# Kernel tuning notes

Hardware: AMD Instinct MI355X
Metric: run time of the kernel (lower is better)

The kernel has to match this reference:

```python
import jax, jax.numpy as jnp
import numpy as np

N_EMBD = 1024
N_HEAD = 16
HEAD_SIZE = N_EMBD // N_HEAD  # 64


def setup_inputs() -> dict:
    key = jax.random.key(0)
    k1, k2, k3, k4 = jax.random.split(key, 4)
    B, T = 4, 4096
    x = jax.random.normal(k1, (B, T, N_EMBD), dtype=jnp.float32)
    scale = 1.0 / np.sqrt(N_EMBD)
    # Linear(n_embd, head_size, bias=False): store as [C, H] so projection is x @ W
    Wk = jax.random.normal(k2, (N_EMBD, HEAD_SIZE), dtype=jnp.float32) * scale
    Wq = jax.random.normal(k3, (N_EMBD, HEAD_SIZE), dtype=jnp.float32) * scale
    Wv = jax.random.normal(k4, (N_EMBD, HEAD_SIZE), dtype=jnp.float32) * scale
    decay_factor = jnp.array([-0.5], dtype=jnp.float32)
    return {"x": x, "Wk": Wk, "Wq": Wq, "Wv": Wv, "decay_factor": decay_factor}


def reference(x, Wk, Wq, Wv, decay_factor):
    B, T, C = x.shape
    H = Wk.shape[1]
    k = x @ Wk  # [B,T,H]
    q = x @ Wq  # [B,T,H]
    v = x @ Wv  # [B,T,H]
    wei = jnp.einsum('bth,bsh->bts', q, k) * (H ** -0.5)  # [B,T,T]
    idx = jnp.arange(T)
    dist = jnp.minimum(idx[None, :] - idx[:, None], 0)  # j - i, clamped max=0
    ripple_bias = dist.astype(x.dtype) * jnp.abs(decay_factor[0])
    wei = wei + ripple_bias[None, :, :]
    causal = idx[None, :] <= idx[:, None]  # tril mask [T,T]
    wei = jnp.where(causal[None, :, :], wei, -jnp.inf)
    wei = jax.nn.softmax(wei, axis=-1)
    return jnp.einsum('bts,bsh->bth', wei, v)
```

## Files before the change

### kernel.cpp

```cpp
#include <hip/hip_runtime.h>

typedef short bf16x8 __attribute__((ext_vector_type(8)));
typedef float f32x4 __attribute__((ext_vector_type(4)));

#define TT 4096
#define CC 1024
#define HH 64
#define MTOT 16384

static __device__ __forceinline__ unsigned short f2bf(float f) {
  unsigned int u = __float_as_uint(f);
  unsigned int r = (u + 0x7FFFu + ((u >> 16) & 1u)) >> 16;
  return (unsigned short)r;
}

static __device__ __forceinline__ unsigned int pack_bf2(float lo, float hi) {
  unsigned int ul = __float_as_uint(lo) + 0x8000u;
  unsigned int uh = __float_as_uint(hi) + 0x8000u;
  return __builtin_amdgcn_perm(uh, ul, 0x07060302u);
}

typedef const __attribute__((address_space(1))) void gvoid;
typedef __attribute__((address_space(3))) void svoid;
static __device__ __forceinline__ void gll16(const void* g, void* l) {
  __builtin_amdgcn_global_load_lds((gvoid*)g, (svoid*)l, 16, 0, 0);
}

#define WAITVM(N) asm volatile("s_waitcnt vmcnt(" #N ")" ::: "memory")

__global__ void prep_wt(const float* __restrict__ Wk, const float* __restrict__ Wq,
                        const float* __restrict__ Wv, unsigned short* __restrict__ Wt) {
  __shared__ float T[64][65];
  const int mat = blockIdx.x >> 4;
  const int kt = blockIdx.x & 15;
  const float* src = (mat == 0) ? Wk : ((mat == 1) ? Wq : Wv);
#pragma unroll
  for (int i = 0; i < 4; ++i) {
    int c = i * 256 + threadIdx.x;
    int row = c >> 4, col = (c & 15) * 4;
    f32x4 v = *(const f32x4*)&src[(size_t)(kt * 64 + row) * HH + col];
    T[col + 0][row] = v[0];
    T[col + 1][row] = v[1];
    T[col + 2][row] = v[2];
    T[col + 3][row] = v[3];
  }
  __syncthreads();
#pragma unroll
  for (int i = 0; i < 2; ++i) {
    int c2 = i * 256 + threadIdx.x;
    int row = c2 >> 3, k0 = (c2 & 7) * 8;
    union { bf16x8 v; unsigned short h[8]; } pk;
#pragma unroll
    for (int j = 0; j < 8; ++j) pk.h[j] = f2bf(T[row][k0 + j]);
    *(bf16x8*)&Wt[(size_t)(mat * 64 + row) * CC + kt * 64 + k0] = pk.v;
  }
}

__global__ __launch_bounds__(512, 2) void proj_kernel(
    const float* __restrict__ x, const unsigned short* __restrict__ Wt,
    unsigned short* __restrict__ kb, unsigned short* __restrict__ qb,
    unsigned short* __restrict__ vt) {
  extern __shared__ __align__(16) char smem[];
  float* Xl = (float*)smem;
  unsigned short* Bl = (unsigned short*)(smem + 49152);

  const int tid = threadIdx.x;
  const int lane = tid & 63;
  const int w = tid >> 6;
  const int r = lane & 15, g = lane >> 4;
  const int rowgrp = w >> 1;
  const int colbase = (w & 1) * 96;
  const int m0 = blockIdx.x * 64;

  const float* xsrcs[2];
#pragma unroll
  for (int j = 0; j < 2; ++j) {
    int c = j * 512 + tid;
    int row = c >> 4, s = c & 15;
    xsrcs[j] = x + (size_t)(m0 + row) * CC + (((s & 8) | ((s & 7) ^ (row & 7))) * 4);
  }
  const unsigned short* bsrcs[3];
#pragma unroll
  for (int j = 0; j < 3; ++j) {
    int cb = j * 512 + tid;
    int row = cb >> 3, s = cb & 7;
    bsrcs[j] = Wt + (size_t)row * CC + ((s ^ (row & 7)) * 8);
  }

  f32x4 acc[6];
#pragma unroll
  for (int n = 0; n < 6; ++n) { f32x4 z = {0.f, 0.f, 0.f, 0.f}; acc[n] = z; }

  auto stage = [&](int t, int buf) {
    float* xb = Xl + buf * 4096;
    unsigned short* bb = Bl + buf * 12288;
#pragma unroll
    for (int j = 0; j < 2; ++j)
      gll16(xsrcs[j] + t * 64, xb + (j * 512 + w * 64) * 4);
#pragma unroll
    for (int j = 0; j < 3; ++j)
      gll16(bsrcs[j] + t * 64, bb + (size_t)(j * 512 + w * 64) * 8);
  };

  const int rr = rowgrp * 16 + r;
  const int rb = rr * 64;
  const int rx = rr & 7;

  auto body = [&](int buf) {
    const float* xb = Xl + buf * 4096;
    const unsigned short* bb = Bl + buf * 12288;
    bf16x8 bfr[2][6];
#pragma unroll
    for (int ks = 0; ks < 2; ++ks)
#pragma unroll
      for (int n = 0; n < 6; ++n) {
        int col = colbase + 16 * n + r;
        bfr[ks][n] = *(const bf16x8*)&bb[col * 64 + (((ks * 4 + g) ^ (col & 7)) * 8)];
      }
#pragma unroll
    for (int ks = 0; ks < 2; ++ks) {
      int s0 = ks * 8 + 2 * g;
      f32x4 v0 = *(const f32x4*)&xb[rb + (((s0 & 8) | ((s0 & 7) ^ rx)) * 4)];
      f32x4 v1 = *(const f32x4*)&xb[rb + ((((s0 + 1) & 8) | (((s0 + 1) & 7) ^ rx)) * 4)];
      union { bf16x8 v; unsigned int u[4]; } af;
      af.u[0] = pack_bf2(v0.x, v0.y);
      af.u[1] = pack_bf2(v0.z, v0.w);
      af.u[2] = pack_bf2(v1.x, v1.y);
      af.u[3] = pack_bf2(v1.z, v1.w);
#pragma unroll
      for (int n = 0; n < 6; ++n)
        acc[n] = __builtin_amdgcn_mfma_f32_16x16x32_bf16(af.v, bfr[ks][n], acc[n], 0, 0, 0);
    }
  };

  stage(0, 0);
  stage(1, 1);

  for (int t = 0; t < 15; ++t) {
    WAITVM(5);
    __builtin_amdgcn_s_barrier();
    if (t + 2 < 16) stage(t + 2, (t + 2) % 3);
    body(t % 3);
  }
  WAITVM(0);
  __builtin_amdgcn_s_barrier();
  body(0);

  float* Vt = (float*)(smem + 73728);
#pragma unroll
  for (int n = 0; n < 6; ++n) {
#pragma unroll
    for (int i = 0; i < 4; ++i) {
      int row = rowgrp * 16 + 4 * g + i;
      int col = colbase + 16 * n + r;
      float val = acc[n][i];
      if (col < 64) {
        kb[(size_t)(m0 + row) * HH + col] = f2bf(val);
      } else if (col < 128) {
        qb[(size_t)(m0 + row) * HH + (col - 64)] = f2bf(val);
      } else {
        Vt[(col - 128) * 65 + row] = val;
      }
    }
  }
  __syncthreads();
  {
    int dim = tid >> 3, t8 = (tid & 7) * 8;
    union { bf16x8 v; unsigned short h[8]; } pk;
#pragma unroll
    for (int j = 0; j < 8; ++j) pk.h[j] = f2bf(Vt[dim * 65 + t8 + j]);
    int b = m0 >> 12;
    int tt = (m0 & (TT - 1)) + t8;
    *(bf16x8*)&vt[(((size_t)b * HH + dim) << 12) + tt] = pk.v;
  }
}

__global__ __launch_bounds__(256, 2) void attn_kernel(
    const unsigned short* __restrict__ qb, const unsigned short* __restrict__ kb,
    const unsigned short* __restrict__ vt, const float* __restrict__ decayp,
    float* __restrict__ out) {
  extern __shared__ __align__(16) char smem[];
  unsigned short* Kl = (unsigned short*)smem;
  unsigned short* Vl = Kl + 16384;
  unsigned short* Pl = Vl + 16384;
  float* Ol = (float*)(smem + 65536);
  float* Ml = (float*)(smem + 65536 + 8704);
  float* Ll = Ml + 32;

  const int tid = threadIdx.x;
  const int lane = tid & 63;
  const int w = tid >> 6;
  const int r = lane & 15, g = lane >> 4;
  const int qh = w & 1;
  const int kvg = w >> 1;

  const int batch = blockIdx.x & 3;
  const int qt = blockIdx.x >> 2;
  const int qbase = qt * 32;
  const int qw = qbase + qh * 16;
  const int qrow = qw + r;

  const float decay = fabsf(decayp[0]);

  const unsigned short* qbb = qb + (size_t)batch * TT * HH;
  const unsigned short* kbb = kb + (size_t)batch * TT * HH;
  const unsigned short* vbb = vt + (size_t)batch * HH * TT;

  const unsigned short* qp = qbb + (size_t)qrow * HH;
  bf16x8 aq0 = *(const bf16x8*)(qp + 8 * g);
  bf16x8 aq1 = *(const bf16x8*)(qp + 32 + 8 * g);

  int t0 = 0;
  if (decay > 1e-8f) {
    float wf = 60.f / decay;
    if (wf < (float)TT) {
      int W = (int)wf + 1;
      int lo = qbase - W;
      if (lo < 0) lo = 0;
      t0 = lo >> 6;
    }
  }
  const int t1 = (qbase + 31) >> 6;
  const int nsteps = (t1 - t0 + 2) >> 1;

  const unsigned short* ksrc[4];
  const unsigned short* vsrc[4];
#pragma unroll
  for (int j = 0; j < 4; ++j) {
    int c = j * 256 + tid;
    int th = c >> 9;
    int cc = c & 511;
    int row = cc >> 3, sl = cc & 7;
    ksrc[j] = kbb + (size_t)((t0 + th) * 64 + row) * HH + ((sl ^ (row & 7)) * 8);
    vsrc[j] = vbb + (size_t)row * TT + (t0 + th) * 64 + ((sl ^ (row & 7)) * 8);
  }

  auto stage = [&](int s, int buf) {
#pragma unroll
    for (int j = 0; j < 4; ++j) {
      gll16(ksrc[j] + (size_t)s * 8192, Kl + buf * 8192 + (j * 256 + w * 64) * 8);
      gll16(vsrc[j] + s * 128, Vl + buf * 8192 + (j * 256 + w * 64) * 8);
    }
  };

  float m = -1e30f, lsum = 0.f;
  f32x4 o[4];
#pragma unroll
  for (int n = 0; n < 4; ++n) { f32x4 z = {0.f, 0.f, 0.f, 0.f}; o[n] = z; }

  stage(0, 0);

  for (int s = 0; s < nsteps; ++s) {
    if (s + 1 < nsteps) { stage(s + 1, (s + 1) & 1); WAITVM(8); }
    else { WAITVM(0); }
    __builtin_amdgcn_s_barrier();

    const int myt = t0 + 2 * s + kvg;
    if (myt <= t1) {
      const unsigned short* Kb = Kl + (s & 1) * 8192 + kvg * 4096;
      const unsigned short* Vb = Vl + (s & 1) * 8192 + kvg * 4096;
      const int kv0 = myt * 64;

      f32x4 sacc[4];
      __builtin_amdgcn_s_setprio(1);
#pragma unroll
      for (int t = 0; t < 4; ++t) {
        f32x4 z = {0.f, 0.f, 0.f, 0.f};
        int kvr = 16 * t + r;
        bf16x8 b0 = *(const bf16x8*)&Kb[kvr * 64 + ((g ^ (kvr & 7)) * 8)];
        bf16x8 b1 = *(const bf16x8*)&Kb[kvr * 64 + (((4 + g) ^ (kvr & 7)) * 8)];
        z = __builtin_amdgcn_mfma_f32_16x16x32_bf16(b0, aq0, z, 0, 0, 0);
        sacc[t] = __builtin_amdgcn_mfma_f32_16x16x32_bf16(b1, aq1, z, 0, 0, 0);
      }
      __builtin_amdgcn_s_setprio(0);

      float p[4][4];
      float rmax = -1e30f;
#pragma unroll
      for (int t = 0; t < 4; ++t)
#pragma unroll
        for (int i = 0; i < 4; ++i) {
          int kv = kv0 + 16 * t + 4 * g + i;
          float sv = sacc[t][i] * 0.125f + decay * (float)(kv - qrow);
          if (kv > qrow) sv = -1e30f;
          p[t][i] = sv;
          rmax = fmaxf(rmax, sv);
        }
      rmax = fmaxf(rmax, __shfl_xor(rmax, 16));
      rmax = fmaxf(rmax, __shfl_xor(rmax, 32));
      float mn = fmaxf(m, rmax);
      float al = __expf(m - mn);
      m = mn;
      float rs = 0.f;
#pragma unroll
      for (int t = 0; t < 4; ++t)
#pragma unroll
        for (int i = 0; i < 4; ++i) {
          float e = __expf(p[t][i] - mn);
          p[t][i] = e;
          rs += e;
        }
      rs += __shfl_xor(rs, 16);
      rs += __shfl_xor(rs, 32);
      lsum = lsum * al + rs;
#pragma unroll
      for (int n = 0; n < 4; ++n) {
        o[n][0] *= al; o[n][1] *= al; o[n][2] *= al; o[n][3] *= al;
      }

      char* P = (char*)(Pl + w * 1024) + r * 128;
#pragma unroll
      for (int t = 0; t < 4; ++t) {
        uint2 u;
        u.x = pack_bf2(p[t][0], p[t][1]);
        u.y = pack_bf2(p[t][2], p[t][3]);
        *(uint2*)(P + ((t ^ (r & 3)) * 32) + g * 8) = u;
      }
      bf16x8 pb0 = *(const bf16x8*)(P + (((g >> 1) ^ (r & 3)) * 32) + (g & 1) * 16);
      bf16x8 pb1 = *(const bf16x8*)(P + ((((g >> 1) + 2) ^ (r & 3)) * 32) + (g & 1) * 16);

      __builtin_amdgcn_s_setprio(1);
#pragma unroll
      for (int n = 0; n < 4; ++n) {
        int dim = 16 * n + r;
        bf16x8 v0 = *(const bf16x8*)&Vb[dim * 64 + ((g ^ (dim & 7)) * 8)];
        bf16x8 v1 = *(const bf16x8*)&Vb[dim * 64 + (((4 + g) ^ (dim & 7)) * 8)];
        o[n] = __builtin_amdgcn_mfma_f32_16x16x32_bf16(v0, pb0, o[n], 0, 0, 0);
        o[n] = __builtin_amdgcn_mfma_f32_16x16x32_bf16(v1, pb1, o[n], 0, 0, 0);
      }
      __builtin_amdgcn_s_setprio(0);
    }
    __builtin_amdgcn_s_barrier();
  }

  const int orow = qh * 16 + r;
  if (kvg == 1) {
    if (lane < 16) { Ml[orow] = m; Ll[orow] = lsum; }
#pragma unroll
    for (int n = 0; n < 4; ++n)
#pragma unroll
      for (int i = 0; i < 4; ++i)
        Ol[orow * 68 + 16 * n + 4 * g + i] = o[n][i];
  }
  __syncthreads();
  if (kvg == 0) {
    float m2 = Ml[orow], l2 = Ll[orow];
    float M = fmaxf(m, m2);
    float e1 = __expf(m - M), e2 = __expf(m2 - M);
    float inv = 1.f / (lsum * e1 + l2 * e2);
#pragma unroll
    for (int n = 0; n < 4; ++n)
#pragma unroll
      for (int i = 0; i < 4; ++i) {
        int d = 16 * n + 4 * g + i;
        Ol[orow * 68 + d] = (o[n][i] * e1 + Ol[orow * 68 + d] * e2) * inv;
      }
  }
  __syncthreads();

  float* ob = out + (size_t)batch * TT * HH;
#pragma unroll
  for (int j = 0; j < 2; ++j) {
    int c = j * 256 + tid;
    int row = c >> 4, q4 = (c & 15) * 4;
    f32x4 vv = *(const f32x4*)&Ol[row * 68 + q4];
    *(f32x4*)&ob[(size_t)(qbase + row) * HH + q4] = vv;
  }
}

extern "C" void kernel_launch(void* const* d_in, const int* in_sizes, int n_in,
                              void* d_out, int out_size, void* d_ws, size_t ws_size,
                              hipStream_t stream) {
  const float* x = (const float*)d_in[0];
  const float* Wk = (const float*)d_in[1];
  const float* Wq = (const float*)d_in[2];
  const float* Wv = (const float*)d_in[3];
  const float* decay = (const float*)d_in[4];
  float* out = (float*)d_out;

  unsigned short* kb = (unsigned short*)d_ws;
  unsigned short* qbw = kb + (size_t)MTOT * HH;
  unsigned short* vt = qbw + (size_t)MTOT * HH;
  unsigned short* Wt = vt + (size_t)MTOT * HH;

  prep_wt<<<dim3(48), dim3(256), 0, stream>>>(Wk, Wq, Wv, Wt);
  proj_kernel<<<dim3(256), dim3(512), 120 * 1024, stream>>>(x, Wt, kb, qbw, vt);
  attn_kernel<<<dim3(512), dim3(256), 74496, stream>>>(qbw, kb, vt, decay, out);
}
```

Baseline: 32.31 us.

## Fuse weight prep, projection and attention into one cooperative kernel

The three separate launches (weight transpose, QKV projection, attention) are merged into a single cooperative kernel with grid-wide syncs between phases. Each 512-thread block now runs two 256-thread attention units side by side instead of using 512 separate blocks. This removes launch overhead and inter-kernel gaps. In exchange, the attention K/V staging loses its double buffering: each step loads, waits for all loads and then syncs. Grid syncs add their own cost.

```diff
diff --git a/kernel.cpp b/kernel.cpp
--- a/kernel.cpp
+++ b/kernel.cpp
@@ -1,4 +1,7 @@
 #include <hip/hip_runtime.h>
+#include <hip/hip_cooperative_groups.h>
+
+namespace cg = cooperative_groups;
 
 typedef short bf16x8 __attribute__((ext_vector_type(8)));
 typedef float f32x4 __attribute__((ext_vector_type(4)));
@@ -28,343 +31,349 @@
 
 #define WAITVM(N) asm volatile("s_waitcnt vmcnt(" #N ")" ::: "memory")
 
-__global__ void prep_wt(const float* __restrict__ Wk, const float* __restrict__ Wq,
-                        const float* __restrict__ Wv, unsigned short* __restrict__ Wt) {
-  __shared__ float T[64][65];
-  const int mat = blockIdx.x >> 4;
-  const int kt = blockIdx.x & 15;
-  const float* src = (mat == 0) ? Wk : ((mat == 1) ? Wq : Wv);
-#pragma unroll
-  for (int i = 0; i < 4; ++i) {
-    int c = i * 256 + threadIdx.x;
-    int row = c >> 4, col = (c & 15) * 4;
-    f32x4 v = *(const f32x4*)&src[(size_t)(kt * 64 + row) * HH + col];
-    T[col + 0][row] = v[0];
-    T[col + 1][row] = v[1];
-    T[col + 2][row] = v[2];
-    T[col + 3][row] = v[3];
-  }
-  __syncthreads();
-#pragma unroll
-  for (int i = 0; i < 2; ++i) {
-    int c2 = i * 256 + threadIdx.x;
-    int row = c2 >> 3, k0 = (c2 & 7) * 8;
-    union { bf16x8 v; unsigned short h[8]; } pk;
-#pragma unroll
-    for (int j = 0; j < 8; ++j) pk.h[j] = f2bf(T[row][k0 + j]);
-    *(bf16x8*)&Wt[(size_t)(mat * 64 + row) * CC + kt * 64 + k0] = pk.v;
-  }
-}
-
-__global__ __launch_bounds__(512, 2) void proj_kernel(
-    const float* __restrict__ x, const unsigned short* __restrict__ Wt,
+__global__ __launch_bounds__(512, 2) void fused_kernel(
+    const float* __restrict__ x, const float* __restrict__ Wk,
+    const float* __restrict__ Wq, const float* __restrict__ Wv,
+    const float* __restrict__ decayp,
     unsigned short* __restrict__ kb, unsigned short* __restrict__ qb,
-    unsigned short* __restrict__ vt) {
+    unsigned short* __restrict__ vt, unsigned short* __restrict__ Wt,
+    float* __restrict__ out) {
   extern __shared__ __align__(16) char smem[];
-  float* Xl = (float*)smem;
-  unsigned short* Bl = (unsigned short*)(smem + 49152);
+  cg::grid_group grid = cg::this_grid();
 
   const int tid = threadIdx.x;
   const int lane = tid & 63;
   const int w = tid >> 6;
   const int r = lane & 15, g = lane >> 4;
-  const int rowgrp = w >> 1;
-  const int colbase = (w & 1) * 96;
-  const int m0 = blockIdx.x * 64;
-
-  const float* xsrcs[2];
-#pragma unroll
-  for (int j = 0; j < 2; ++j) {
-    int c = j * 512 + tid;
-    int row = c >> 4, s = c & 15;
-    xsrcs[j] = x + (size_t)(m0 + row) * CC + (((s & 8) | ((s & 7) ^ (row & 7))) * 4);
+
+  if (blockIdx.x < 48) {
+    float* T = (float*)smem;
+    const int mat = blockIdx.x >> 4;
+    const int kt = blockIdx.x & 15;
+    const float* src = (mat == 0) ? Wk : ((mat == 1) ? Wq : Wv);
+#pragma unroll
+    for (int i = 0; i < 2; ++i) {
+      int c = i * 512 + tid;
+      int row = c >> 4, col = (c & 15) * 4;
+      f32x4 v = *(const f32x4*)&src[(size_t)(kt * 64 + row) * HH + col];
+      T[(col + 0) * 65 + row] = v[0];
+      T[(col + 1) * 65 + row] = v[1];
+      T[(col + 2) * 65 + row] = v[2];
+      T[(col + 3) * 65 + row] = v[3];
+    }
+    __syncthreads();
+    {
+      int row = tid >> 3, k0 = (tid & 7) * 8;
+      union { bf16x8 v; unsigned short h[8]; } pk;
+#pragma unroll
+      for (int j = 0; j < 8; ++j) pk.h[j] = f2bf(T[row * 65 + k0 + j]);
+      *(bf16x8*)&Wt[(size_t)(mat * 64 + row) * CC + kt * 64 + k0] = pk.v;
+    }
   }
-  const unsigned short* bsrcs[3];
-#pragma unroll
-  for (int j = 0; j < 3; ++j) {
-    int cb = j * 512 + tid;
-    int row = cb >> 3, s = cb & 7;
-    bsrcs[j] = Wt + (size_t)row * CC + ((s ^ (row & 7)) * 8);
+  grid.sync();
+
+  {
+    float* Xl = (float*)smem;
+    unsigned short* Bl = (unsigned short*)(smem + 49152);
+
+    const int rowgrp = w >> 1;
+    const int colbase = (w & 1) * 96;
+    const int m0 = blockIdx.x * 64;
+
+    const float* xsrcs[2];
+#pragma unroll
+    for (int j = 0; j < 2; ++j) {
+      int c = j * 512 + tid;
+      int row = c >> 4, s = c & 15;
+      xsrcs[j] = x + (size_t)(m0 + row) * CC + (((s & 8) | ((s & 7) ^ (row & 7))) * 4);
+    }
+    const unsigned short* bsrcs[3];
+#pragma unroll
+    for (int j = 0; j < 3; ++j) {
+      int cb = j * 512 + tid;
+      int row = cb >> 3, s = cb & 7;
+      bsrcs[j] = Wt + (size_t)row * CC + ((s ^ (row & 7)) * 8);
+    }
+
+    f32x4 acc[6];
+#pragma unroll
+    for (int n = 0; n < 6; ++n) { f32x4 z = {0.f, 0.f, 0.f, 0.f}; acc[n] = z; }
+
+    auto stage = [&](int t, int buf) {
+      float* xb = Xl + buf * 4096;
+      unsigned short* bb = Bl + buf * 12288;
+#pragma unroll
+      for (int j = 0; j < 2; ++j)
+        gll16(xsrcs[j] + t * 64, xb + (j * 512 + w * 64) * 4);
+#pragma unroll
+      for (int j = 0; j < 3; ++j)
+        gll16(bsrcs[j] + t * 64, bb + (size_t)(j * 512 + w * 64) * 8);
+    };
+
+    const int rr = rowgrp * 16 + r;
+    const int rb = rr * 64;
+    const int rx = rr & 7;
+
+    auto body = [&](int buf) {
+      const float* xb = Xl + buf * 4096;
+      const unsigned short* bb = Bl + buf * 12288;
+      bf16x8 bfr[2][6];
+#pragma unroll
+      for (int ks = 0; ks < 2; ++ks)
+#pragma unroll
+        for (int n = 0; n < 6; ++n) {
+          int col = colbase + 16 * n + r;
+          bfr[ks][n] = *(const bf16x8*)&bb[col * 64 + (((ks * 4 + g) ^ (col & 7)) * 8)];
+        }
+#pragma unroll
+      for (int ks = 0; ks < 2; ++ks) {
+        int s0 = ks * 8 + 2 * g;
+        f32x4 v0 = *(const f32x4*)&xb[rb + (((s0 & 8) | ((s0 & 7) ^ rx)) * 4)];
+        f32x4 v1 = *(const f32x4*)&xb[rb + ((((s0 + 1) & 8) | (((s0 + 1) & 7) ^ rx)) * 4)];
+        union { bf16x8 v; unsigned int u[4]; } af;
+        af.u[0] = pack_bf2(v0.x, v0.y);
+        af.u[1] = pack_bf2(v0.z, v0.w);
+        af.u[2] = pack_bf2(v1.x, v1.y);
+        af.u[3] = pack_bf2(v1.z, v1.w);
+#pragma unroll
+        for (int n = 0; n < 6; ++n)
+          acc[n] = __builtin_amdgcn_mfma_f32_16x16x32_bf16(af.v, bfr[ks][n], acc[n], 0, 0, 0);
+      }
+    };
+
+    stage(0, 0);
+    stage(1, 1);
+
+    for (int t = 0; t < 15; ++t) {
+      WAITVM(5);
+      __builtin_amdgcn_s_barrier();
+      if (t + 2 < 16) stage(t + 2, (t + 2) % 3);
+      body(t % 3);
+    }
+    WAITVM(0);
+    __builtin_amdgcn_s_barrier();
+    body(0);
+
+    float* Vt = (float*)(smem + 73728);
+#pragma unroll
+    for (int n = 0; n < 6; ++n) {
+#pragma unroll
+      for (int i = 0; i < 4; ++i) {
+        int row = rowgrp * 16 + 4 * g + i;
+        int col = colbase + 16 * n + r;
+        float val = acc[n][i];
+        if (col < 64) {
+          kb[(size_t)(m0 + row) * HH + col] = f2bf(val);
+        } else if (col < 128) {
+          qb[(size_t)(m0 + row) * HH + (col - 64)] = f2bf(val);
+        } else {
+          Vt[(col - 128) * 65 + row] = val;
+        }
+      }
+    }
+    __syncthreads();
+    {
+      int dim = tid >> 3, t8 = (tid & 7) * 8;
+      union { bf16x8 v; unsigned short h[8]; } pk;
+#pragma unroll
+      for (int j = 0; j < 8; ++j) pk.h[j] = f2bf(Vt[dim * 65 + t8 + j]);
+      int b = m0 >> 12;
+      int tt = (m0 & (TT - 1)) + t8;
+      *(bf16x8*)&vt[(((size_t)b * HH + dim) << 12) + tt] = pk.v;
+    }
   }
-
-  f32x4 acc[6];
-#pragma unroll
-  for (int n = 0; n < 6; ++n) { f32x4 z = {0.f, 0.f, 0.f, 0.f}; acc[n] = z; }
-
-  auto stage = [&](int t, int buf) {
-    float* xb = Xl + buf * 4096;
-    unsigned short* bb = Bl + buf * 12288;
-#pragma unroll
-    for (int j = 0; j < 2; ++j)
-      gll16(xsrcs[j] + t * 64, xb + (j * 512 + w * 64) * 4);
-#pragma unroll
-    for (int j = 0; j < 3; ++j)
-      gll16(bsrcs[j] + t * 64, bb + (size_t)(j * 512 + w * 64) * 8);
-  };
-
-  const int rr = rowgrp * 16 + r;
-  const int rb = rr * 64;
-  const int rx = rr & 7;
-
-  auto body = [&](int buf) {
-    const float* xb = Xl + buf * 4096;
-    const unsigned short* bb = Bl + buf * 12288;
-    bf16x8 bfr[2][6];
-#pragma unroll
-    for (int ks = 0; ks < 2; ++ks)
-#pragma unroll
-      for (int n = 0; n < 6; ++n) {
-        int col = colbase + 16 * n + r;
-        bfr[ks][n] = *(const bf16x8*)&bb[col * 64 + (((ks * 4 + g) ^ (col & 7)) * 8)];
+  grid.sync();
+
+  {
+    unsigned short* KlA = (unsigned short*)smem;
+    unsigned short* VlA = (unsigned short*)(smem + 32768);
+    unsigned short* PlA = (unsigned short*)(smem + 65536);
+    float* OlA = (float*)(smem + 81920);
+    float* MlA = (float*)(smem + 99328);
+    float* LlA = (float*)(smem + 99584);
+
+    const int half = w >> 2;
+    const int wl = w & 3;
+    const int htid = tid & 255;
+    const int u = blockIdx.x * 2 + half;
+    const int batch = u & 3;
+    const int qt = u >> 2;
+    const int qbase = qt * 32;
+    const int qh = wl & 1;
+    const int kvg = wl >> 1;
+    const int qw = qbase + qh * 16;
+    const int qrow = qw + r;
+
+    const float decay = fabsf(decayp[0]);
+
+    const unsigned short* qbb = qb + (size_t)batch * TT * HH;
+    const unsigned short* kbb = kb + (size_t)batch * TT * HH;
+    const unsigned short* vbb = vt + (size_t)batch * HH * TT;
+
+    const unsigned short* qp = qbb + (size_t)qrow * HH;
+    bf16x8 aq0 = *(const bf16x8*)(qp + 8 * g);
+    bf16x8 aq1 = *(const bf16x8*)(qp + 32 + 8 * g);
+
+    int t0 = 0;
+    if (decay > 1e-8f) {
+      float wf = 60.f / decay;
+      if (wf < (float)TT) {
+        int W = (int)wf + 1;
+        int lo = qbase - W;
+        if (lo < 0) lo = 0;
+        t0 = lo >> 6;
       }
-#pragma unroll
-    for (int ks = 0; ks < 2; ++ks) {
-      int s0 = ks * 8 + 2 * g;
-      f32x4 v0 = *(const f32x4*)&xb[rb + (((s0 & 8) | ((s0 & 7) ^ rx)) * 4)];
-      f32x4 v1 = *(const f32x4*)&xb[rb + ((((s0 + 1) & 8) | (((s0 + 1) & 7) ^ rx)) * 4)];
-      union { bf16x8 v; unsigned int u[4]; } af;
-      af.u[0] = pack_bf2(v0.x, v0.y);
-      af.u[1] = pack_bf2(v0.z, v0.w);
-      af.u[2] = pack_bf2(v1.x, v1.y);
-      af.u[3] = pack_bf2(v1.z, v1.w);
-#pragma unroll
-      for (int n = 0; n < 6; ++n)
-        acc[n] = __builtin_amdgcn_mfma_f32_16x16x32_bf16(af.v, bfr[ks][n], acc[n], 0, 0, 0);
-    }
-  };
-
-  stage(0, 0);
-  stage(1, 1);
-
-  for (int t = 0; t < 15; ++t) {
-    WAITVM(5);
-    __builtin_amdgcn_s_barrier();
-    if (t + 2 < 16) stage(t + 2, (t + 2) % 3);
-    body(t % 3);
-  }
-  WAITVM(0);
-  __builtin_amdgcn_s_barrier();
-  body(0);
-
-  float* Vt = (float*)(smem + 73728);
-#pragma unroll
-  for (int n = 0; n < 6; ++n) {
-#pragma unroll
-    for (int i = 0; i < 4; ++i) {
-      int row = rowgrp * 16 + 4 * g + i;
-      int col = colbase + 16 * n + r;
-      float val = acc[n][i];
-      if (col < 64) {
-        kb[(size_t)(m0 + row) * HH + col] = f2bf(val);
-      } else if (col < 128) {
-        qb[(size_t)(m0 + row) * HH + (col - 64)] = f2bf(val);
-      } else {
-        Vt[(col - 128) * 65 + row] = val;
+    }
+    const int t1 = (qbase + 31) >> 6;
+    const int nsteps = (t1 - t0 + 2) >> 1;
+
+    const unsigned short* ksrc[4];
+    const unsigned short* vsrc[4];
+#pragma unroll
+    for (int j = 0; j < 4; ++j) {
+      int c = j * 256 + htid;
+      int th = c >> 9;
+      int cc = c & 511;
+      int row = cc >> 3, sl = cc & 7;
+      ksrc[j] = kbb + (size_t)((t0 + th) * 64 + row) * HH + ((sl ^ (row & 7)) * 8);
+      vsrc[j] = vbb + (size_t)row * TT + (t0 + th) * 64 + ((sl ^ (row & 7)) * 8);
+    }
+
+    unsigned short* Kh = KlA + half * 8192;
+    unsigned short* Vh = VlA + half * 8192;
+
+    auto stageC = [&](int s) {
+#pragma unroll
+      for (int j = 0; j < 4; ++j) {
+        gll16(ksrc[j] + (size_t)s * 8192, Kh + (j * 256 + wl * 64) * 8);
+        gll16(vsrc[j] + s * 128, Vh + (j * 256 + wl * 64) * 8);
       }
-    }
-  }
-  __syncthreads();
-  {
-    int dim = tid >> 3, t8 = (tid & 7) * 8;
-    union { bf16x8 v; unsigned short h[8]; } pk;
-#pragma unroll
-    for (int j = 0; j < 8; ++j) pk.h[j] = f2bf(Vt[dim * 65 + t8 + j]);
-    int b = m0 >> 12;
-    int tt = (m0 & (TT - 1)) + t8;
-    *(bf16x8*)&vt[(((size_t)b * HH + dim) << 12) + tt] = pk.v;
-  }
-}
-
-__global__ __launch_bounds__(256, 2) void attn_kernel(
-    const unsigned short* __restrict__ qb, const unsigned short* __restrict__ kb,
-    const unsigned short* __restrict__ vt, const float* __restrict__ decayp,
-    float* __restrict__ out) {
-  extern __shared__ __align__(16) char smem[];
-  unsigned short* Kl = (unsigned short*)smem;
-  unsigned short* Vl = Kl + 16384;
-  unsigned short* Pl = Vl + 16384;
-  float* Ol = (float*)(smem + 65536);
-  float* Ml = (float*)(smem + 65536 + 8704);
-  float* Ll = Ml + 32;
-
-  const int tid = threadIdx.x;
-  const int lane = tid & 63;
-  const int w = tid >> 6;
-  const int r = lane & 15, g = lane >> 4;
-  const int qh = w & 1;
-  const int kvg = w >> 1;
-
-  const int batch = blockIdx.x & 3;
-  const int qt = blockIdx.x >> 2;
-  const int qbase = qt * 32;
-  const int qw = qbase + qh * 16;
-  const int qrow = qw + r;
-
-  const float decay = fabsf(decayp[0]);
-
-  const unsigned short* qbb = qb + (size_t)batch * TT * HH;
-  const unsigned short* kbb = kb + (size_t)batch * TT * HH;
-  const unsigned short* vbb = vt + (size_t)batch * HH * TT;
-
-  const unsigned short* qp = qbb + (size_t)qrow * HH;
-  bf16x8 aq0 = *(const bf16x8*)(qp + 8 * g);
-  bf16x8 aq1 = *(const bf16x8*)(qp + 32 + 8 * g);
-
-  int t0 = 0;
-  if (decay > 1e-8f) {
-    float wf = 60.f / decay;
-    if (wf < (float)TT) {
-      int W = (int)wf + 1;
-      int lo = qbase - W;
-      if (lo < 0) lo = 0;
-      t0 = lo >> 6;
-    }
-  }
-  const int t1 = (qbase + 31) >> 6;
-  const int nsteps = (t1 - t0 + 2) >> 1;
-
-  const unsigned short* ksrc[4];
-  const unsigned short* vsrc[4];
-#pragma unroll
-  for (int j = 0; j < 4; ++j) {
-    int c = j * 256 + tid;
-    int th = c >> 9;
-    int cc = c & 511;
-    int row = cc >> 3, sl = cc & 7;
-    ksrc[j] = kbb + (size_t)((t0 + th) * 64 + row) * HH + ((sl ^ (row & 7)) * 8);
-    vsrc[j] = vbb + (size_t)row * TT + (t0 + th) * 64 + ((sl ^ (row & 7)) * 8);
-  }
-
-  auto stage = [&](int s, int buf) {
-#pragma unroll
-    for (int j = 0; j < 4; ++j) {
-      gll16(ksrc[j] + (size_t)s * 8192, Kl + buf * 8192 + (j * 256 + w * 64) * 8);
-      gll16(vsrc[j] + s * 128, Vl + buf * 8192 + (j * 256 + w * 64) * 8);
-    }
-  };
-
-  float m = -1e30f, lsum = 0.f;
-  f32x4 o[4];
-#pragma unroll
-  for (int n = 0; n < 4; ++n) { f32x4 z = {0.f, 0.f, 0.f, 0.f}; o[n] = z; }
-
-  stage(0, 0);
-
-  for (int s = 0; s < nsteps; ++s) {
-    if (s + 1 < nsteps) { stage(s + 1, (s + 1) & 1); WAITVM(8); }
-    else { WAITVM(0); }
-    __builtin_amdgcn_s_barrier();
-
-    const int myt = t0 + 2 * s + kvg;
-    if (myt <= t1) {
-      const unsigned short* Kb = Kl + (s & 1) * 8192 + kvg * 4096;
-      const unsigned short* Vb = Vl + (s & 1) * 8192 + kvg * 4096;
-      const int kv0 = myt * 64;
-
-      f32x4 sacc[4];
-      __builtin_amdgcn_s_setprio(1);
-#pragma unroll
-      for (int t = 0; t < 4; ++t) {
-        f32x4 z = {0.f, 0.f, 0.f, 0.f};
-        int kvr = 16 * t + r;
-        bf16x8 b0 = *(const bf16x8*)&Kb[kvr * 64 + ((g ^ (kvr & 7)) * 8)];
-        bf16x8 b1 = *(const bf16x8*)&Kb[kvr * 64 + (((4 + g) ^ (kvr & 7)) * 8)];
-        z = __builtin_amdgcn_mfma_f32_16x16x32_bf16(b0, aq0, z, 0, 0, 0);
-        sacc[t] = __builtin_amdgcn_mfma_f32_16x16x32_bf16(b1, aq1, z, 0, 0, 0);
+    };
+
+    float m = -1e30f, lsum = 0.f;
+    f32x4 o[4];
+#pragma unroll
+    for (int n = 0; n < 4; ++n) { f32x4 z = {0.f, 0.f, 0.f, 0.f}; o[n] = z; }
+
+    for (int s = 0; s < nsteps; ++s) {
+      stageC(s);
+      WAITVM(0);
+      __syncthreads();
+
+      const int myt = t0 + 2 * s + kvg;
+      if (myt <= t1) {
+        const unsigned short* Kb = Kh + kvg * 4096;
+        const unsigned short* Vb = Vh + kvg * 4096;
+        const int kv0 = myt * 64;
+
+        f32x4 sacc[4];
+        __builtin_amdgcn_s_setprio(1);
+#pragma unroll
+        for (int t = 0; t < 4; ++t) {
+          f32x4 z = {0.f, 0.f, 0.f, 0.f};
+          int kvr = 16 * t + r;
+          bf16x8 b0 = *(const bf16x8*)&Kb[kvr * 64 + ((g ^ (kvr & 7)) * 8)];
+          bf16x8 b1 = *(const bf16x8*)&Kb[kvr * 64 + (((4 + g) ^ (kvr & 7)) * 8)];
+          z = __builtin_amdgcn_mfma_f32_16x16x32_bf16(b0, aq0, z, 0, 0, 0);
+          sacc[t] = __builtin_amdgcn_mfma_f32_16x16x32_bf16(b1, aq1, z, 0, 0, 0);
+        }
+        __builtin_amdgcn_s_setprio(0);
+
+        float p[4][4];
+        float rmax = -1e30f;
+#pragma unroll
+        for (int t = 0; t < 4; ++t)
+#pragma unroll
+          for (int i = 0; i < 4; ++i) {
+            int kv = kv0 + 16 * t + 4 * g + i;
+            float sv = sacc[t][i] * 0.125f + decay * (float)(kv - qrow);
+            if (kv > qrow) sv = -1e30f;
+            p[t][i] = sv;
+            rmax = fmaxf(rmax, sv);
+          }
+        rmax = fmaxf(rmax, __shfl_xor(rmax, 16));
+        rmax = fmaxf(rmax, __shfl_xor(rmax, 32));
+        float mn = fmaxf(m, rmax);
+        float al = __expf(m - mn);
+        m = mn;
+        float rs = 0.f;
+#pragma unroll
+        for (int t = 0; t < 4; ++t)
+#pragma unroll
+          for (int i = 0; i < 4; ++i) {
+            float e = __expf(p[t][i] - mn);
+            p[t][i] = e;
+            rs += e;
+          }
+        rs += __shfl_xor(rs, 16);
+        rs += __shfl_xor(rs, 32);
+        lsum = lsum * al + rs;
+#pragma unroll
+        for (int n = 0; n < 4; ++n) {
+          o[n][0] *= al; o[n][1] *= al; o[n][2] *= al; o[n][3] *= al;
+        }
+
+        char* P = (char*)(PlA + (half * 4 + wl) * 1024) + r * 128;
+#pragma unroll
+        for (int t = 0; t < 4; ++t) {
+          uint2 uu;
+          uu.x = pack_bf2(p[t][0], p[t][1]);
+          uu.y = pack_bf2(p[t][2], p[t][3]);
+          *(uint2*)(P + ((t ^ (r & 3)) * 32) + g * 8) = uu;
+        }
+        bf16x8 pb0 = *(const bf16x8*)(P + (((g >> 1) ^ (r & 3)) * 32) + (g & 1) * 16);
+        bf16x8 pb1 = *(const bf16x8*)(P + ((((g >> 1) + 2) ^ (r & 3)) * 32) + (g & 1) * 16);
+
+        __builtin_amdgcn_s_setprio(1);
+#pragma unroll
+        for (int n = 0; n < 4; ++n) {
+          int dim = 16 * n + r;
+          bf16x8 v0 = *(const bf16x8*)&Vb[dim * 64 + ((g ^ (dim & 7)) * 8)];
+          bf16x8 v1 = *(const bf16x8*)&Vb[dim * 64 + (((4 + g) ^ (dim & 7)) * 8)];
+          o[n] = __builtin_amdgcn_mfma_f32_16x16x32_bf16(v0, pb0, o[n], 0, 0, 0);
+          o[n] = __builtin_amdgcn_mfma_f32_16x16x32_bf16(v1, pb1, o[n], 0, 0, 0);
+        }
+        __builtin_amdgcn_s_setprio(0);
       }
-      __builtin_amdgcn_s_setprio(0);
-
-      float p[4][4];
-      float rmax = -1e30f;
-#pragma unroll
-      for (int t = 0; t < 4; ++t)
+      __syncthreads();
+    }
+
+    const int orow = qh * 16 + r;
+    float* Olh = OlA + half * 2176;
+    float* Mlh = MlA + half * 32;
+    float* Llh = LlA + half * 32;
+    if (kvg == 1) {
+      if (lane < 16) { Mlh[orow] = m; Llh[orow] = lsum; }
+#pragma unroll
+      for (int n = 0; n < 4; ++n)
+#pragma unroll
+        for (int i = 0; i < 4; ++i)
+          Olh[orow * 68 + 16 * n + 4 * g + i] = o[n][i];
+    }
+    __syncthreads();
+    if (kvg == 0) {
+      float m2 = Mlh[orow], l2 = Llh[orow];
+      float M = fmaxf(m, m2);
+      float e1 = __expf(m - M), e2 = __expf(m2 - M);
+      float inv = 1.f / (lsum * e1 + l2 * e2);
+#pragma unroll
+      for (int n = 0; n < 4; ++n)
 #pragma unroll
         for (int i = 0; i < 4; ++i) {
-          int kv = kv0 + 16 * t + 4 * g + i;
-          float sv = sacc[t][i] * 0.125f + decay * (float)(kv - qrow);
-          if (kv > qrow) sv = -1e30f;
-          p[t][i] = sv;
-          rmax = fmaxf(rmax, sv);
-        }
-      rmax = fmaxf(rmax, __shfl_xor(rmax, 16));
-      rmax = fmaxf(rmax, __shfl_xor(rmax, 32));
-      float mn = fmaxf(m, rmax);
-      float al = __expf(m - mn);
-      m = mn;
-      float rs = 0.f;
-#pragma unroll
-      for (int t = 0; t < 4; ++t)
-#pragma unroll
-        for (int i = 0; i < 4; ++i) {
-          float e = __expf(p[t][i] - mn);
-          p[t][i] = e;
-          rs += e;
-        }
-      rs += __shfl_xor(rs, 16);
-      rs += __shfl_xor(rs, 32);
-      lsum = lsum * al + rs;
-#pragma unroll
-      for (int n = 0; n < 4; ++n) {
-        o[n][0] *= al; o[n][1] *= al; o[n][2] *= al; o[n][3] *= al;
-      }
-
-      char* P = (char*)(Pl + w * 1024) + r * 128;
-#pragma unroll
-      for (int t = 0; t < 4; ++t) {
-        uint2 u;
-        u.x = pack_bf2(p[t][0], p[t][1]);
-        u.y = pack_bf2(p[t][2], p[t][3]);
-        *(uint2*)(P + ((t ^ (r & 3)) * 32) + g * 8) = u;
-      }
-      bf16x8 pb0 = *(const bf16x8*)(P + (((g >> 1) ^ (r & 3)) * 32) + (g & 1) * 16);
-      bf16x8 pb1 = *(const bf16x8*)(P + ((((g >> 1) + 2) ^ (r & 3)) * 32) + (g & 1) * 16);
-
-      __builtin_amdgcn_s_setprio(1);
-#pragma unroll
-      for (int n = 0; n < 4; ++n) {
-        int dim = 16 * n + r;
-        bf16x8 v0 = *(const bf16x8*)&Vb[dim * 64 + ((g ^ (dim & 7)) * 8)];
-        bf16x8 v1 = *(const bf16x8*)&Vb[dim * 64 + (((4 + g) ^ (dim & 7)) * 8)];
-        o[n] = __builtin_amdgcn_mfma_f32_16x16x32_bf16(v0, pb0, o[n], 0, 0, 0);
-        o[n] = __builtin_amdgcn_mfma_f32_16x16x32_bf16(v1, pb1, o[n], 0, 0, 0);
-      }
-      __builtin_amdgcn_s_setprio(0);
-    }
-    __builtin_amdgcn_s_barrier();
-  }
-
-  const int orow = qh * 16 + r;
-  if (kvg == 1) {
-    if (lane < 16) { Ml[orow] = m; Ll[orow] = lsum; }
-#pragma unroll
-    for (int n = 0; n < 4; ++n)
-#pragma unroll
-      for (int i = 0; i < 4; ++i)
-        Ol[orow * 68 + 16 * n + 4 * g + i] = o[n][i];
-  }
-  __syncthreads();
-  if (kvg == 0) {
-    float m2 = Ml[orow], l2 = Ll[orow];
-    float M = fmaxf(m, m2);
-    float e1 = __expf(m - M), e2 = __expf(m2 - M);
-    float inv = 1.f / (lsum * e1 + l2 * e2);
-#pragma unroll
-    for (int n = 0; n < 4; ++n)
-#pragma unroll
-      for (int i = 0; i < 4; ++i) {
-        int d = 16 * n + 4 * g + i;
-        Ol[orow * 68 + d] = (o[n][i] * e1 + Ol[orow * 68 + d] * e2) * inv;
-      }
-  }
-  __syncthreads();
-
-  float* ob = out + (size_t)batch * TT * HH;
-#pragma unroll
-  for (int j = 0; j < 2; ++j) {
-    int c = j * 256 + tid;
-    int row = c >> 4, q4 = (c & 15) * 4;
-    f32x4 vv = *(const f32x4*)&Ol[row * 68 + q4];
-    *(f32x4*)&ob[(size_t)(qbase + row) * HH + q4] = vv;
+          int d = 16 * n + 4 * g + i;
+          Olh[orow * 68 + d] = (o[n][i] * e1 + Olh[orow * 68 + d] * e2) * inv;
+        }
+    }
+    __syncthreads();
+
+    float* ob = out + (size_t)batch * TT * HH;
+#pragma unroll
+    for (int j = 0; j < 2; ++j) {
+      int c = j * 256 + htid;
+      int row = c >> 4, q4 = (c & 15) * 4;
+      f32x4 vv = *(const f32x4*)&Olh[row * 68 + q4];
+      *(f32x4*)&ob[(size_t)(qbase + row) * HH + q4] = vv;
+    }
   }
 }
 
@@ -380,10 +389,21 @@
 
   unsigned short* kb = (unsigned short*)d_ws;
   unsigned short* qbw = kb + (size_t)MTOT * HH;
-  unsigned short* vt = qbw + (size_t)MTOT * HH;
-  unsigned short* Wt = vt + (size_t)MTOT * HH;
-
-  prep_wt<<<dim3(48), dim3(256), 0, stream>>>(Wk, Wq, Wv, Wt);
-  proj_kernel<<<dim3(256), dim3(512), 120 * 1024, stream>>>(x, Wt, kb, qbw, vt);
-  attn_kernel<<<dim3(512), dim3(256), 74496, stream>>>(qbw, kb, vt, decay, out);
+  unsigned short* vtw = qbw + (size_t)MTOT * HH;
+  unsigned short* Wt = vtw + (size_t)MTOT * HH;
+
+  void* args[10];
+  args[0] = (void*)&x;
+  args[1] = (void*)&Wk;
+  args[2] = (void*)&Wq;
+  args[3] = (void*)&Wv;
+  args[4] = (void*)&decay;
+  args[5] = (void*)&kb;
+  args[6] = (void*)&qbw;
+  args[7] = (void*)&vtw;
+  args[8] = (void*)&Wt;
+  args[9] = (void*)&out;
+
+  hipLaunchCooperativeKernel(reinterpret_cast<void*>(fused_kernel),
+                             dim3(256), dim3(512), args, 120 * 1024, stream);
 }
```

Result: slower. 97.05 us (+200.3%).
